# Performance work log

Hardware: AMD Instinct MI355X
Metric: run time of the kernel (lower is better)

## Reference

```python
import jax, jax.numpy as jnp
import numpy as np

NIBBLE_ZERO = 8  # int4 zero-point (symmetric around 8 for unsigned nibble storage)


def _dequant(w_packed, w_scales):
    # w_packed: [out, in//2] int32 holding uint8 bytes, two 4-bit values each.
    low = w_packed & 0xF            # first nibble -> even input positions
    high = (w_packed >> 4) & 0xF    # second nibble -> odd input positions
    out_f = w_packed.shape[0]
    # interleave nibbles along the input dim: [out, in//2, 2] -> [out, in]
    q = jnp.stack([low, high], axis=-1).reshape(out_f, -1)
    return (q.astype(w_scales.dtype) - NIBBLE_ZERO) * w_scales[:, None]  # [out, in]


def setup_inputs() -> dict:
    key = jax.random.key(0)
    k1, k2, k3, k4 = jax.random.split(key, 4)
    N, IN, OUT = 4096, 4096, 4096
    x = jax.random.normal(k1, (N, IN), dtype=jnp.float32)
    w_packed = jax.random.randint(k2, (OUT, IN // 2), 0, 256, dtype=jnp.int32)
    w_scales = jax.random.uniform(k3, (OUT,), dtype=jnp.float32, minval=0.01, maxval=0.05)
    bias = jax.random.normal(k4, (OUT,), dtype=jnp.float32)
    return {"x": x, "w_packed": w_packed, "w_scales": w_scales, "bias": bias}


def reference(x, w_packed, w_scales, bias):
    W = _dequant(w_packed, w_scales)          # [out, in]
    return jnp.einsum('ni,oi->no', x, W) + bias  # [N, out]
```

## Files before the change

kernel.cpp:

```cpp
#include <hip/hip_runtime.h>
#include <hip/hip_bf16.h>


typedef __attribute__((ext_vector_type(8))) __bf16 bf16x8;
typedef __attribute__((ext_vector_type(4))) float f32x4;

#define GLOBAL_AS __attribute__((address_space(1)))
#define LDS_AS __attribute__((address_space(3)))

#define BM 256
#define BN 256
#define BK 64

__device__ inline unsigned short f32_to_bf16(float f) {
    unsigned int u = __float_as_uint(f);
    unsigned int r = (u + 0x7FFFu + ((u >> 16) & 1u)) >> 16;
    return (unsigned short)r;
}

__global__ void prep(const float* __restrict__ x, unsigned short* __restrict__ xb,
                     const int* __restrict__ wp, unsigned short* __restrict__ wb,
                     int n8x, int n4w) {
    const int stride = gridDim.x * blockDim.x;
    const int total = n8x + n4w;
    for (int i = blockIdx.x * blockDim.x + threadIdx.x; i < total; i += stride) {
        if (i < n8x) {
            float4 a = ((const float4*)x)[2 * i];
            float4 b = ((const float4*)x)[2 * i + 1];
            union { unsigned short h[8]; uint4 u; } o;
            o.h[0] = f32_to_bf16(a.x); o.h[1] = f32_to_bf16(a.y);
            o.h[2] = f32_to_bf16(a.z); o.h[3] = f32_to_bf16(a.w);
            o.h[4] = f32_to_bf16(b.x); o.h[5] = f32_to_bf16(b.y);
            o.h[6] = f32_to_bf16(b.z); o.h[7] = f32_to_bf16(b.w);
            ((uint4*)xb)[i] = o.u;
        } else {
            int k = i - n8x;
            int4 v = ((const int4*)wp)[k];
            int vals[4] = {v.x, v.y, v.z, v.w};
            union { unsigned short h[8]; uint4 u; } o;
#pragma unroll
            for (int t = 0; t < 4; ++t) {
                o.h[2 * t]     = f32_to_bf16((float)((vals[t] & 0xF) - 8));
                o.h[2 * t + 1] = f32_to_bf16((float)(((vals[t] >> 4) & 0xF) - 8));
            }
            ((uint4*)wb)[k] = o.u;
        }
    }
}

template<int K, int N>
__global__ __launch_bounds__(512, 2) void gemm_bt(
    const unsigned short* __restrict__ A,
    const unsigned short* __restrict__ B,
    const float* __restrict__ scales,
    const float* __restrict__ bias,
    float* __restrict__ C,
    int GY)
{
    constexpr int NT = K / BK;
    __shared__ __align__(16) unsigned short lds[65536];

    const int tid  = threadIdx.x;
    const int wave = tid >> 6;
    const int lane = tid & 63;
    const int wm = wave >> 2;
    const int wn = wave & 3;

    const int bid = blockIdx.x;
    const int chunk = gridDim.x >> 3;
    const int sw = (bid & 7) * chunk + (bid >> 3);
    const int bx = sw / GY;
    const int by = sw - bx * GY;
    const int m0 = by * BM;
    const int n0 = bx * BN;

    const int am = lane & 15;
    const int aq = lane >> 4;
    const int cb = ((aq ^ (am & 7)) << 4);

    int aoff[8], boff[4];
#pragma unroll
    for (int i = 0; i < 8; ++i) {
        int r = (2 * i + wm) * 16 + am;
        aoff[i] = ((i < 4) ? 0 : 16384) + (r & 127) * 128 + cb;
    }
#pragma unroll
    for (int j = 0; j < 4; ++j) {
        int r = (4 * j + wn) * 16 + am;
        boff[j] = 32768 + ((j < 2) ? 0 : 16384) + (r & 127) * 128 + cb;
    }

    const int sch = tid & 7;
    const int r0 = tid >> 3;
    const int r1 = (512 + tid) >> 3;
    const size_t g0 = (size_t)r0 * K + (size_t)((sch ^ (r0 & 7)) * 8);
    const size_t g1 = (size_t)r1 * K + (size_t)((sch ^ (r1 & 7)) * 8);
    const int d0 = tid * 8;
    const int d1 = (512 + tid) * 8;

    const unsigned short* Abase = A + (size_t)m0 * K;
    const unsigned short* Bbase = B + (size_t)n0 * K;

    f32x4 acc[8][4];
#pragma unroll
    for (int i = 0; i < 8; ++i)
#pragma unroll
        for (int j = 0; j < 4; ++j)
            acc[i][j] = (f32x4){0.f, 0.f, 0.f, 0.f};

    const char* ldsB = (const char*)lds;
    bf16x8 af[4][2], bf[2][2];

#define STAGE(gbase, half, kcol, uoff)                                            \
    do {                                                                          \
        const unsigned short* _g = (gbase) + (size_t)((half) * 128) * K + (kcol); \
        __builtin_amdgcn_global_load_lds((const GLOBAL_AS void*)(_g + g0),        \
            (LDS_AS void*)(lds + (uoff) + d0), 16, 0, 0);                         \
        __builtin_amdgcn_global_load_lds((const GLOBAL_AS void*)(_g + g1),        \
            (LDS_AS void*)(lds + (uoff) + d1), 16, 0, 0);                         \
    } while (0)

#define LDA(mh, OB)                                                               \
    _Pragma("unroll") for (int i2 = 0; i2 < 4; ++i2) {                            \
        af[i2][0] = *(const bf16x8*)(ldsB + (OB) + aoff[(mh) * 4 + i2]);          \
        af[i2][1] = *(const bf16x8*)(ldsB + (OB) + (aoff[(mh) * 4 + i2] ^ 64));   \
    }

#define LDB(nh, OB)                                                               \
    _Pragma("unroll") for (int j2 = 0; j2 < 2; ++j2) {                            \
        bf[j2][0] = *(const bf16x8*)(ldsB + (OB) + boff[(nh) * 2 + j2]);          \
        bf[j2][1] = *(const bf16x8*)(ldsB + (OB) + (boff[(nh) * 2 + j2] ^ 64));   \
    }

#define BAR_LG()                                                                  \
    __builtin_amdgcn_s_barrier();                                                 \
    asm volatile("s_waitcnt lgkmcnt(0)" ::: "memory");                            \
    __builtin_amdgcn_sched_barrier(0)

#define MFMA_Q(mh, nh)                                                            \
    _Pragma("unroll") for (int i2 = 0; i2 < 4; ++i2)                              \
    _Pragma("unroll") for (int j2 = 0; j2 < 2; ++j2) {                            \
        acc[(mh) * 4 + i2][(nh) * 2 + j2] = __builtin_amdgcn_mfma_f32_16x16x32_bf16( \
            af[i2][0], bf[j2][0], acc[(mh) * 4 + i2][(nh) * 2 + j2], 0, 0, 0);    \
        acc[(mh) * 4 + i2][(nh) * 2 + j2] = __builtin_amdgcn_mfma_f32_16x16x32_bf16( \
            af[i2][1], bf[j2][1], acc[(mh) * 4 + i2][(nh) * 2 + j2], 0, 0, 0);    \
    }

#define GROUP(OB, OUS, OUSo, t)                                                   \
    {                                                                             \
        const int kn1 = (((t) + 1 < NT) ? (t) + 1 : NT - 1) * BK;                 \
        const int kn2 = (((t) + 2 < NT) ? (t) + 2 : NT - 1) * BK;                 \
                                                             \
        LDA(0, OB); LDB(0, OB);                                                   \
        STAGE(Bbase, 0, kn1, (OUSo) + 16384);                                     \
        BAR_LG();                                                                 \
        __builtin_amdgcn_s_setprio(1); MFMA_Q(0, 0); __builtin_amdgcn_s_setprio(0); \
        __builtin_amdgcn_s_barrier();                                             \
                                                             \
        LDB(1, OB);                                                               \
        STAGE(Abase, 1, kn1, (OUSo) + 8192);                                      \
        BAR_LG();                                                                 \
        __builtin_amdgcn_s_setprio(1); MFMA_Q(0, 1); __builtin_amdgcn_s_setprio(0); \
        __builtin_amdgcn_s_barrier();                                             \
                                                             \
        LDA(1, OB);                                                               \
        STAGE(Abase, 0, kn2, (OUS) + 0);                                          \
        BAR_LG();                                                                 \
        __builtin_amdgcn_s_setprio(1); MFMA_Q(1, 1); __builtin_amdgcn_s_setprio(0); \
        __builtin_amdgcn_s_barrier();                                             \
                                                             \
        LDB(0, OB);                                                               \
        STAGE(Bbase, 1, kn2, (OUS) + 24576);                                      \
        asm volatile("s_waitcnt vmcnt(4)" ::: "memory");                          \
        BAR_LG();                                                                 \
        __builtin_amdgcn_s_setprio(1); MFMA_Q(1, 0); __builtin_amdgcn_s_setprio(0); \
        __builtin_amdgcn_s_barrier();                                             \
    }

    STAGE(Abase, 0, 0, 0);
    STAGE(Bbase, 1, 0, 24576);
    STAGE(Bbase, 0, 0, 16384);
    STAGE(Abase, 1, 0, 8192);
    STAGE(Abase, 0, BK, 32768);
    STAGE(Bbase, 1, BK, 32768 + 24576);
    asm volatile("s_waitcnt vmcnt(4)" ::: "memory");
    __builtin_amdgcn_s_barrier();

    for (int t = 0; t < NT; t += 2) {
        GROUP(0, 0, 32768, t);
        GROUP(65536, 32768, 0, t + 1);
    }

    const int cq = lane >> 4;
    const int cc = lane & 15;
#pragma unroll
    for (int j = 0; j < 4; ++j) {
        const int col = n0 + (4 * j + wn) * 16 + cc;
        const float s = scales[col];
        const float b = bias[col];
#pragma unroll
        for (int i = 0; i < 8; ++i) {
            const int rowb = m0 + (2 * i + wm) * 16 + cq * 4;
#pragma unroll
            for (int r = 0; r < 4; ++r) {
                C[(size_t)(rowb + r) * N + col] = acc[i][j][r] * s + b;
            }
        }
    }
#undef STAGE
#undef LDA
#undef LDB
#undef BAR_LG
#undef MFMA_Q
#undef GROUP
}

__global__ void naive_kernel(const float* __restrict__ x, const int* __restrict__ wp,
                             const float* __restrict__ sc, const float* __restrict__ bs,
                             float* __restrict__ out, int NR, int OUTF, int INF) {
    int idx = blockIdx.x * 256 + threadIdx.x;
    if (idx >= NR * OUTF) return;
    int n = idx / OUTF, o = idx - n * OUTF;
    const float* xr = x + (size_t)n * INF;
    const int* wr = wp + (size_t)o * (INF / 2);
    float acc = 0.f;
    for (int c = 0; c < INF / 2; ++c) {
        int v = wr[c];
        acc += xr[2 * c] * (float)((v & 0xF) - 8) + xr[2 * c + 1] * (float)(((v >> 4) & 0xF) - 8);
    }
    out[idx] = acc * sc[o] + bs[o];
}

extern "C" void kernel_launch(void* const* d_in, const int* in_sizes, int n_in,
                              void* d_out, int out_size, void* d_ws, size_t ws_size,
                              hipStream_t stream) {
    const float* x      = (const float*)d_in[0];
    const int*   wp     = (const int*)d_in[1];
    const float* scales = (const float*)d_in[2];
    const float* bias   = (const float*)d_in[3];
    float* out = (float*)d_out;

    const int OUTF = in_sizes[2];
    const int INF  = (2 * in_sizes[1]) / OUTF;
    const int NR   = in_sizes[0] / INF;

    unsigned short* xb = (unsigned short*)d_ws;
    unsigned short* wb = xb + (size_t)NR * INF;
    const size_t need = ((size_t)NR * INF + (size_t)OUTF * INF) * sizeof(unsigned short);

    const int GX = OUTF / BN;
    const int GY = NR / BM;

    if (ws_size >= need && INF == 4096 && OUTF == 4096 && (NR % BM) == 0
        && ((GX * GY) % 8) == 0
        && (in_sizes[0] % 8) == 0 && (in_sizes[1] % 4) == 0) {
        prep<<<2048, 256, 0, stream>>>(x, xb, wp, wb, in_sizes[0] / 8, in_sizes[1] / 4);
        gemm_bt<4096, 4096><<<GX * GY, 512, 0, stream>>>(xb, wb, scales, bias, out, GY);
    } else {
        int total = NR * OUTF;
        naive_kernel<<<(total + 255) / 256, 256, 0, stream>>>(x, wp, scales, bias, out, NR, OUTF, INF);
    }
}
```

Measured before the change: 264.1 us.

## Double-buffer LDS fragment registers to prefetch next quadrant during MFMA

Fragment registers for A and B are split into two sets. LDS reads for the next quadrant, including the first quadrant of the next K tile, are issued after the barrier and before the current MFMA block. The aim is to overlap LDS read latency with matrix math instead of waiting on lgkmcnt before each MFMA block. This raises VGPR pressure and depends on the reordered reads seeing the correct LDS buffer contents.

Result: slower. 342.6 us (+29.7%).

```diff
diff --git a/kernel.cpp b/kernel.cpp
--- a/kernel.cpp
+++ b/kernel.cpp
@@ -109,7 +109,8 @@
             acc[i][j] = (f32x4){0.f, 0.f, 0.f, 0.f};
 
     const char* ldsB = (const char*)lds;
-    bf16x8 af[4][2], bf[2][2];
+    bf16x8 af[2][4][2];
+    bf16x8 bfr[2][2][2];
 
 #define STAGE(gbase, half, kcol, uoff)                                            \
     do {                                                                          \
@@ -120,16 +121,16 @@
             (LDS_AS void*)(lds + (uoff) + d1), 16, 0, 0);                         \
     } while (0)
 
-#define LDA(mh, OB)                                                               \
+#define LDA_S(S, mh, OBb)                                                         \
     _Pragma("unroll") for (int i2 = 0; i2 < 4; ++i2) {                            \
-        af[i2][0] = *(const bf16x8*)(ldsB + (OB) + aoff[(mh) * 4 + i2]);          \
-        af[i2][1] = *(const bf16x8*)(ldsB + (OB) + (aoff[(mh) * 4 + i2] ^ 64));   \
-    }
-
-#define LDB(nh, OB)                                                               \
+        af[S][i2][0] = *(const bf16x8*)(ldsB + (OBb) + aoff[(mh) * 4 + i2]);      \
+        af[S][i2][1] = *(const bf16x8*)(ldsB + (OBb) + (aoff[(mh) * 4 + i2] ^ 64)); \
+    }
+
+#define LDB_S(S, nh, OBb)                                                         \
     _Pragma("unroll") for (int j2 = 0; j2 < 2; ++j2) {                            \
-        bf[j2][0] = *(const bf16x8*)(ldsB + (OB) + boff[(nh) * 2 + j2]);          \
-        bf[j2][1] = *(const bf16x8*)(ldsB + (OB) + (boff[(nh) * 2 + j2] ^ 64));   \
+        bfr[S][j2][0] = *(const bf16x8*)(ldsB + (OBb) + boff[(nh) * 2 + j2]);     \
+        bfr[S][j2][1] = *(const bf16x8*)(ldsB + (OBb) + (boff[(nh) * 2 + j2] ^ 64)); \
     }
 
 #define BAR_LG()                                                                  \
@@ -137,43 +138,43 @@
     asm volatile("s_waitcnt lgkmcnt(0)" ::: "memory");                            \
     __builtin_amdgcn_sched_barrier(0)
 
-#define MFMA_Q(mh, nh)                                                            \
+#define MFMA_Q(AS, BS, mh, nh)                                                    \
     _Pragma("unroll") for (int i2 = 0; i2 < 4; ++i2)                              \
     _Pragma("unroll") for (int j2 = 0; j2 < 2; ++j2) {                            \
         acc[(mh) * 4 + i2][(nh) * 2 + j2] = __builtin_amdgcn_mfma_f32_16x16x32_bf16( \
-            af[i2][0], bf[j2][0], acc[(mh) * 4 + i2][(nh) * 2 + j2], 0, 0, 0);    \
+            af[AS][i2][0], bfr[BS][j2][0], acc[(mh) * 4 + i2][(nh) * 2 + j2], 0, 0, 0); \
         acc[(mh) * 4 + i2][(nh) * 2 + j2] = __builtin_amdgcn_mfma_f32_16x16x32_bf16( \
-            af[i2][1], bf[j2][1], acc[(mh) * 4 + i2][(nh) * 2 + j2], 0, 0, 0);    \
-    }
-
-#define GROUP(OB, OUS, OUSo, t)                                                   \
+            af[AS][i2][1], bfr[BS][j2][1], acc[(mh) * 4 + i2][(nh) * 2 + j2], 0, 0, 0); \
+    }
+
+#define GROUP(OB, OUS, OUSo, t, SX, SY)                                           \
     {                                                                             \
         const int kn1 = (((t) + 1 < NT) ? (t) + 1 : NT - 1) * BK;                 \
         const int kn2 = (((t) + 2 < NT) ? (t) + 2 : NT - 1) * BK;                 \
-                                                             \
-        LDA(0, OB); LDB(0, OB);                                                   \
+                                              \
         STAGE(Bbase, 0, kn1, (OUSo) + 16384);                                     \
         BAR_LG();                                                                 \
-        __builtin_amdgcn_s_setprio(1); MFMA_Q(0, 0); __builtin_amdgcn_s_setprio(0); \
-        __builtin_amdgcn_s_barrier();                                             \
-                                                             \
-        LDB(1, OB);                                                               \
+        LDA_S(SY, 1, OB);                           \
+        __builtin_amdgcn_s_setprio(1); MFMA_Q(SX, 0, 0, 0); __builtin_amdgcn_s_setprio(0); \
+        __builtin_amdgcn_s_barrier();                                             \
+                                              \
         STAGE(Abase, 1, kn1, (OUSo) + 8192);                                      \
         BAR_LG();                                                                 \
-        __builtin_amdgcn_s_setprio(1); MFMA_Q(0, 1); __builtin_amdgcn_s_setprio(0); \
-        __builtin_amdgcn_s_barrier();                                             \
-                                                             \
-        LDA(1, OB);                                                               \
+        LDB_S(1, 1, OB);                            \
+        __builtin_amdgcn_s_setprio(1); MFMA_Q(SY, 0, 1, 0); __builtin_amdgcn_s_setprio(0); \
+        __builtin_amdgcn_s_barrier();                                             \
+                                              \
         STAGE(Abase, 0, kn2, (OUS) + 0);                                          \
         BAR_LG();                                                                 \
-        __builtin_amdgcn_s_setprio(1); MFMA_Q(1, 1); __builtin_amdgcn_s_setprio(0); \
-        __builtin_amdgcn_s_barrier();                                             \
-                                                             \
-        LDB(0, OB);                                                               \
+        __builtin_amdgcn_s_setprio(1); MFMA_Q(SY, 1, 1, 1); __builtin_amdgcn_s_setprio(0); \
+        __builtin_amdgcn_s_barrier();                                             \
+         \
         STAGE(Bbase, 1, kn2, (OUS) + 24576);                                      \
         asm volatile("s_waitcnt vmcnt(4)" ::: "memory");                          \
         BAR_LG();                                                                 \
-        __builtin_amdgcn_s_setprio(1); MFMA_Q(1, 0); __builtin_amdgcn_s_setprio(0); \
+        LDA_S(SY, 0, (OUSo) * 2);                                                 \
+        LDB_S(0, 0, (OUSo) * 2);                                                  \
+        __builtin_amdgcn_s_setprio(1); MFMA_Q(SX, 1, 0, 1); __builtin_amdgcn_s_setprio(0); \
         __builtin_amdgcn_s_barrier();                                             \
     }
 
@@ -185,10 +186,12 @@
     STAGE(Bbase, 1, BK, 32768 + 24576);
     asm volatile("s_waitcnt vmcnt(4)" ::: "memory");
     __builtin_amdgcn_s_barrier();
+    LDA_S(0, 0, 0);
+    LDB_S(0, 0, 0);
 
     for (int t = 0; t < NT; t += 2) {
-        GROUP(0, 0, 32768, t);
-        GROUP(65536, 32768, 0, t + 1);
+        GROUP(0,     0,     32768, t,     0, 1);
+        GROUP(65536, 32768, 0,     t + 1, 1, 0);
     }
 
     const int cq = lane >> 4;
@@ -208,8 +211,8 @@
         }
     }
 #undef STAGE
-#undef LDA
-#undef LDB
+#undef LDA_S
+#undef LDB_S
 #undef BAR_LG
 #undef MFMA_Q
 #undef GROUP
```
